# Kernel tuning notes

Measured on AMD Instinct MI355X. Metric: run time of the kernel, lower is better.

Reference implementation:

```python
import jax, jax.numpy as jnp
import numpy as np

EPS = 1e-8


def _cdist(a, b):
    # a: [B,N,3], b: [B,M,3] -> euclidean distances [B,N,M]
    a2 = jnp.sum(a * a, axis=-1)[:, :, None]          # [B,N,1]
    b2 = jnp.sum(b * b, axis=-1)[:, None, :]          # [B,1,M]
    ab = jnp.einsum('bnd,bmd->bnm', a, b)             # [B,N,M]
    d2 = jnp.maximum(a2 + b2 - 2.0 * ab, 0.0)
    return jnp.sqrt(d2)


def setup_inputs() -> dict:
    key = jax.random.key(0)
    ks = jax.random.split(key, 8)
    B, N, M, C1, C2 = 16, 4096, 1024, 128, 256
    Cin = C1 + C2  # 384
    H1, H2 = 256, 128
    return {
        'xyz1': jax.random.normal(ks[0], (B, N, 3), dtype=jnp.float32),
        'xyz2': jax.random.normal(ks[1], (B, M, 3), dtype=jnp.float32),
        'points1': jax.random.normal(ks[2], (B, C1, N), dtype=jnp.float32),
        'points2': jax.random.normal(ks[3], (B, C2, M), dtype=jnp.float32),
        'W1': jax.random.normal(ks[4], (H1, Cin), dtype=jnp.float32) * (1.0 / np.sqrt(Cin)),
        'b1': jnp.zeros((H1,), dtype=jnp.float32),
        'W2': jax.random.normal(ks[5], (H2, H1), dtype=jnp.float32) * (1.0 / np.sqrt(H1)),
        'b2': jnp.zeros((H2,), dtype=jnp.float32),
    }


def reference(xyz1, xyz2, points1, points2, W1, b1, W2, b2):
    # inverse-distance weighted interpolation over ALL M source points
    dist = _cdist(xyz1, xyz2) + EPS                   # [B,N,M]
    inv = 1.0 / dist
    weight = inv / jnp.sum(inv, axis=-1, keepdims=True)
    # interpolated features: [B,N,M] @ [B,M,C2] -> [B,C2,N]
    interpolated = jnp.einsum('bnm,bcm->bcn', weight, points2)
    new_points = jnp.concatenate([points1, interpolated], axis=1)  # [B,C1+C2,N]
    # 1x1 Conv1d MLP with ReLU
    h = jax.nn.relu(jnp.einsum('oc,bcn->bon', W1, new_points) + b1[None, :, None])
    out = jax.nn.relu(jnp.einsum('oc,bcn->bon', W2, h) + b2[None, :, None])
    return out
```

## Files before the change

### kernel.cpp

```cpp
#include <hip/hip_runtime.h>
#include <math.h>

#define BBATCH 16
#define NPTS   4096
#define MPTS   1024
#define C1c    128
#define C2c    256
#define CINc   384
#define H1c    256
#define H2c    128
#define TN     64

typedef _Float16 f16x8 __attribute__((ext_vector_type(8)));
typedef _Float16 f16x4 __attribute__((ext_vector_type(4)));
typedef float    f32x4 __attribute__((ext_vector_type(4)));

#define LDP2 40
#define LDXc 408
#define LDH  264

#define OFF_XYZ2 0
#define OFF_P2   12288
#define SMEM_BYTES 53248

#define WS_P2H  0
#define WS_W1H  (BBATCH * C2c * MPTS)
#define WS_W2H  (WS_W1H + H1c * CINc)
#define WS_F16_TOTAL (WS_W2H + H2c * H1c)

__global__ __launch_bounds__(256) void cvt_f16(
    const float* __restrict__ p2, const float* __restrict__ W1,
    const float* __restrict__ W2, _Float16* __restrict__ ws)
{
    const int NP2 = BBATCH * C2c * MPTS / 4;
    const int NW1 = H1c * CINc / 4;
    const int i = blockIdx.x * 256 + threadIdx.x;
    float4 v; _Float16* dst;
    if (i < NP2)            { v = ((const float4*)p2)[i];            dst = ws + WS_P2H + (size_t)i * 4; }
    else if (i < NP2 + NW1) { int j = i - NP2; v = ((const float4*)W1)[j]; dst = ws + WS_W1H + (size_t)j * 4; }
    else                    { int j = i - NP2 - NW1; v = ((const float4*)W2)[j]; dst = ws + WS_W2H + (size_t)j * 4; }
    f16x4 h;
    h[0] = (_Float16)v.x; h[1] = (_Float16)v.y; h[2] = (_Float16)v.z; h[3] = (_Float16)v.w;
    *(f16x4*)dst = h;
}

template <bool F16P>
__global__ __launch_bounds__(256, 3) void fp_mfma2(
    const float* __restrict__ xyz1, const float* __restrict__ xyz2,
    const float* __restrict__ p1,   const float* __restrict__ p2,
    const float* __restrict__ W1,   const float* __restrict__ b1v,
    const float* __restrict__ W2,   const float* __restrict__ b2v,
    const _Float16* __restrict__ p2h, const _Float16* __restrict__ W1h,
    const _Float16* __restrict__ W2h,
    float* __restrict__ out)
{
    __shared__ __align__(16) char smem[SMEM_BYTES];
    float*    s_xyz2 = (float*)(smem + OFF_XYZ2);
    _Float16* s_p2   = (_Float16*)(smem + OFF_P2);
    _Float16* s_X    = (_Float16*)smem;
    _Float16* s_H    = (_Float16*)smem;

    const int tid  = threadIdx.x;
    const int w    = tid >> 6;
    const int L    = tid & 63;
    const int quad = L >> 4;
    const int l16  = L & 15;

    const int id = blockIdx.x;
    const int b  = (id & 7) * 2 + ((id >> 3) & 1);
    const int n0 = (id >> 4) * TN;

    const float*    __restrict__ p2b  = p2  + (size_t)b * C2c * MPTS;
    const _Float16* __restrict__ p2hb = F16P ? (p2h + (size_t)b * C2c * MPTS) : (const _Float16*)nullptr;
    const float*    __restrict__ z2b  = xyz2 + (size_t)b * MPTS * 3;

    for (int i = tid; i < MPTS * 3; i += 256) s_xyz2[i] = z2b[i];

    {
    }
    const float x1x = xyz1[((size_t)b * NPTS + n0 + w * 16 + l16) * 3 + 0];
    const float x1y = xyz1[((size_t)b * NPTS + n0 + w * 16 + l16) * 3 + 1];
    const float x1z = xyz1[((size_t)b * NPTS + n0 + w * 16 + l16) * 3 + 2];

    f32x4 acc[16];
    #pragma unroll
    for (int ct = 0; ct < 16; ++ct) acc[ct] = (f32x4){0.f, 0.f, 0.f, 0.f};
    f32x4 accS = (f32x4){0.f, 0.f, 0.f, 0.f};

    f16x8 onesv;
    #pragma unroll
    for (int i = 0; i < 8; ++i) onesv[i] = (_Float16)1.0f;

    f16x8  stg16[4];
    float4 stg32[8];

    if (F16P) {
        #pragma unroll
        for (int r = 0; r < 4; ++r)
            stg16[r] = *(const f16x8*)(p2hb + (size_t)(r * 64 + (tid >> 2)) * MPTS + (tid & 3) * 8);
    } else {
        #pragma unroll
        for (int r = 0; r < 8; ++r)
            stg32[r] = *(const float4*)(p2b + (size_t)(r * 32 + (tid >> 3)) * MPTS + (tid & 7) * 4);
    }

    __syncthreads();

    #pragma unroll 2
    for (int s = 0; s < 32; ++s) {
        _Float16* buf = s_p2 + (s & 1) * (C2c * LDP2);
        if (F16P) {
            #pragma unroll
            for (int r = 0; r < 4; ++r)
                *(f16x8*)(buf + (r * 64 + (tid >> 2)) * LDP2 + (tid & 3) * 8) = stg16[r];
        } else {
            #pragma unroll
            for (int r = 0; r < 8; ++r) {
                const float4 v = stg32[r];
                f16x4 h;
                h[0] = (_Float16)v.x; h[1] = (_Float16)v.y; h[2] = (_Float16)v.z; h[3] = (_Float16)v.w;
                *(f16x4*)(buf + (r * 32 + (tid >> 3)) * LDP2 + (tid & 7) * 4) = h;
            }
        }
        __syncthreads();

        if (s + 1 < 32) {
            const int m1 = (s + 1) * 32;
            if (F16P) {
                #pragma unroll
                for (int r = 0; r < 4; ++r)
                    stg16[r] = *(const f16x8*)(p2hb + (size_t)(r * 64 + (tid >> 2)) * MPTS + m1 + (tid & 3) * 8);
            } else {
                #pragma unroll
                for (int r = 0; r < 8; ++r)
                    stg32[r] = *(const float4*)(p2b + (size_t)(r * 32 + (tid >> 3)) * MPTS + m1 + (tid & 7) * 4);
            }
        }

        f32x4 zr[6];
        {
            const float* zp = s_xyz2 + (s * 32 + quad * 8) * 3;
            #pragma unroll
            for (int j = 0; j < 6; ++j) zr[j] = *(const f32x4*)(zp + j * 4);
        }
        const float* zv = (const float*)zr;
        f16x8 af;
        #pragma unroll
        for (int i = 0; i < 8; ++i) {
            const float dx = x1x - zv[3 * i + 0];
            const float dy = x1y - zv[3 * i + 1];
            const float dz = x1z - zv[3 * i + 2];
            const float d2 = fmaf(dx, dx, fmaf(dy, dy, fmaf(dz, dz, 1e-12f)));
            af[i] = (_Float16)__builtin_amdgcn_rsqf(d2);
        }

        accS = __builtin_amdgcn_mfma_f32_16x16x32_f16(af, onesv, accS, 0, 0, 0);
        const _Float16* bbase = buf + l16 * LDP2 + quad * 8;
        #pragma unroll
        for (int ct = 0; ct < 16; ++ct) {
            const f16x8 bf = *(const f16x8*)(bbase + ct * (16 * LDP2));
            acc[ct] = __builtin_amdgcn_mfma_f32_16x16x32_f16(af, bf, acc[ct], 0, 0, 0);
        }
    }

    __syncthreads();

    float rn[4];
    #pragma unroll
    for (int r = 0; r < 4; ++r) rn[r] = 1.0f / accS[r];

    #pragma unroll
    for (int ct = 0; ct < 16; ++ct)
        #pragma unroll
        for (int r = 0; r < 4; ++r)
            s_X[(w * 16 + quad * 4 + r) * LDXc + 128 + ct * 16 + l16] =
                (_Float16)(acc[ct][r] * rn[r]);

    {
        const float* p1b = p1 + (size_t)b * C1c * NPTS + n0;
        #pragma unroll
        for (int cc = 0; cc < 8; ++cc) {
            const int c = w * 32 + cc * 4;
            f16x4 v;
            v[0] = (_Float16)p1b[(size_t)(c + 0) * NPTS + L];
            v[1] = (_Float16)p1b[(size_t)(c + 1) * NPTS + L];
            v[2] = (_Float16)p1b[(size_t)(c + 2) * NPTS + L];
            v[3] = (_Float16)p1b[(size_t)(c + 3) * NPTS + L];
            *(f16x4*)(&s_X[L * LDXc + c]) = v;
        }
    }
    __syncthreads();

    f32x4 hacc[4][4];
    #pragma unroll
    for (int ct = 0; ct < 4; ++ct)
        #pragma unroll
        for (int nt = 0; nt < 4; ++nt)
            hacc[ct][nt] = (f32x4){0.f, 0.f, 0.f, 0.f};

    #pragma unroll 2
    for (int kc = 0; kc < 12; ++kc) {
        f16x8 af[4];
        if (F16P) {
            const _Float16* wp = W1h + (size_t)(w * 64 + l16) * CINc + kc * 32 + quad * 8;
            #pragma unroll
            for (int ct = 0; ct < 4; ++ct) af[ct] = *(const f16x8*)(wp + ct * (16 * CINc));
        } else {
            const float* wp = W1 + (size_t)(w * 64 + l16) * CINc + kc * 32 + quad * 8;
            #pragma unroll
            for (int ct = 0; ct < 4; ++ct) {
                const float4 a0 = *(const float4*)(wp + ct * (16 * CINc));
                const float4 a1 = *(const float4*)(wp + ct * (16 * CINc) + 4);
                f16x8 h;
                h[0] = (_Float16)a0.x; h[1] = (_Float16)a0.y; h[2] = (_Float16)a0.z; h[3] = (_Float16)a0.w;
                h[4] = (_Float16)a1.x; h[5] = (_Float16)a1.y; h[6] = (_Float16)a1.z; h[7] = (_Float16)a1.w;
                af[ct] = h;
            }
        }
        #pragma unroll
        for (int nt = 0; nt < 4; ++nt) {
            const f16x8 bf = *(const f16x8*)(&s_X[(nt * 16 + l16) * LDXc + kc * 32 + quad * 8]);
            #pragma unroll
            for (int ct = 0; ct < 4; ++ct)
                hacc[ct][nt] = __builtin_amdgcn_mfma_f32_16x16x32_f16(af[ct], bf, hacc[ct][nt], 0, 0, 0);
        }
    }

    __syncthreads();

    {
        f32x4 bb[4];
        #pragma unroll
        for (int ct = 0; ct < 4; ++ct)
            bb[ct] = *(const f32x4*)(b1v + w * 64 + ct * 16 + quad * 4);
        #pragma unroll
        for (int ct = 0; ct < 4; ++ct)
            #pragma unroll
            for (int nt = 0; nt < 4; ++nt) {
                const f32x4 v = hacc[ct][nt];
                f16x4 hv;
                hv[0] = (_Float16)fmaxf(v[0] + bb[ct][0], 0.f);
                hv[1] = (_Float16)fmaxf(v[1] + bb[ct][1], 0.f);
                hv[2] = (_Float16)fmaxf(v[2] + bb[ct][2], 0.f);
                hv[3] = (_Float16)fmaxf(v[3] + bb[ct][3], 0.f);
                *(f16x4*)(&s_H[(nt * 16 + l16) * LDH + w * 64 + ct * 16 + quad * 4]) = hv;
            }
    }
    __syncthreads();

    f32x4 oacc[2][4];
    #pragma unroll
    for (int ct = 0; ct < 2; ++ct)
        #pragma unroll
        for (int nt = 0; nt < 4; ++nt)
            oacc[ct][nt] = (f32x4){0.f, 0.f, 0.f, 0.f};

    #pragma unroll 2
    for (int oc = 0; oc < 8; ++oc) {
        f16x8 af2[2];
        if (F16P) {
            const _Float16* wp = W2h + (size_t)(w * 32 + l16) * H1c + oc * 32 + quad * 8;
            #pragma unroll
            for (int ct = 0; ct < 2; ++ct) af2[ct] = *(const f16x8*)(wp + ct * (16 * H1c));
        } else {
            const float* wp = W2 + (size_t)(w * 32 + l16) * H1c + oc * 32 + quad * 8;
            #pragma unroll
            for (int ct = 0; ct < 2; ++ct) {
                const float4 a0 = *(const float4*)(wp + ct * (16 * H1c));
                const float4 a1 = *(const float4*)(wp + ct * (16 * H1c) + 4);
                f16x8 h;
                h[0] = (_Float16)a0.x; h[1] = (_Float16)a0.y; h[2] = (_Float16)a0.z; h[3] = (_Float16)a0.w;
                h[4] = (_Float16)a1.x; h[5] = (_Float16)a1.y; h[6] = (_Float16)a1.z; h[7] = (_Float16)a1.w;
                af2[ct] = h;
            }
        }
        #pragma unroll
        for (int nt = 0; nt < 4; ++nt) {
            const f16x8 bf = *(const f16x8*)(&s_H[(nt * 16 + l16) * LDH + oc * 32 + quad * 8]);
            #pragma unroll
            for (int ct = 0; ct < 2; ++ct)
                oacc[ct][nt] = __builtin_amdgcn_mfma_f32_16x16x32_f16(af2[ct], bf, oacc[ct][nt], 0, 0, 0);
        }
    }

    {
        f32x4 bb2[2];
        #pragma unroll
        for (int ct = 0; ct < 2; ++ct)
            bb2[ct] = *(const f32x4*)(b2v + w * 32 + ct * 16 + quad * 4);
        #pragma unroll
        for (int ct = 0; ct < 2; ++ct)
            #pragma unroll
            for (int nt = 0; nt < 4; ++nt) {
                float* op = out + ((size_t)b * H2c + w * 32 + ct * 16 + quad * 4) * NPTS
                                + n0 + nt * 16 + l16;
                #pragma unroll
                for (int j = 0; j < 4; ++j)
                    op[(size_t)j * NPTS] = fmaxf(oacc[ct][nt][j] + bb2[ct][j], 0.f);
            }
    }
}

extern "C" void kernel_launch(void* const* d_in, const int* in_sizes, int n_in,
                              void* d_out, int out_size, void* d_ws, size_t ws_size,
                              hipStream_t stream) {
    (void)in_sizes; (void)n_in; (void)out_size;
    const float* xyz1 = (const float*)d_in[0];
    const float* xyz2 = (const float*)d_in[1];
    const float* p1   = (const float*)d_in[2];
    const float* p2   = (const float*)d_in[3];
    const float* W1   = (const float*)d_in[4];
    const float* b1   = (const float*)d_in[5];
    const float* W2   = (const float*)d_in[6];
    const float* b2   = (const float*)d_in[7];
    float* out = (float*)d_out;

    const bool useh = (ws_size >= (size_t)WS_F16_TOTAL * 2);
    dim3 grid(BBATCH * (NPTS / TN));
    dim3 block(256);
    if (useh) {
        _Float16* ws = (_Float16*)d_ws;
        const int ncvt = (BBATCH * C2c * MPTS + H1c * CINc + H2c * H1c) / 4;
        cvt_f16<<<dim3(ncvt / 256), dim3(256), 0, stream>>>(p2, W1, W2, ws);
        fp_mfma2<true><<<grid, block, 0, stream>>>(xyz1, xyz2, p1, p2, W1, b1, W2, b2,
                                                   ws + WS_P2H, ws + WS_W1H, ws + WS_W2H, out);
    } else {
        fp_mfma2<false><<<grid, block, 0, stream>>>(xyz1, xyz2, p1, p2, W1, b1, W2, b2,
                                                    nullptr, nullptr, nullptr, out);
    }
}
```

Before: 198.0 us.

## Swap MFMA operand roles: stream points2 from global, stage inverse weights in LDS

The interpolation GEMM is reorganized so each wave owns 64 output channels and loads its points2 A-fragments straight from global memory into registers, double-buffered. Only the 64x32 inverse-distance tile goes through LDS, which replaces staging the 256x32 points2 tile there. The row sums move from an extra MFMA against a ones vector to scalar accumulation plus a small LDS reduction. LDS traffic per step drops, at the cost of more redundant global/L2 reads of points2 across waves and blocks and a less coalesced access pattern.

```diff
diff --git a/kernel.cpp b/kernel.cpp
--- a/kernel.cpp
+++ b/kernel.cpp
@@ -15,12 +15,14 @@
 typedef _Float16 f16x4 __attribute__((ext_vector_type(4)));
 typedef float    f32x4 __attribute__((ext_vector_type(4)));
 
-#define LDP2 40
+#define LDI  40
 #define LDXc 408
 #define LDH  264
 
-#define OFF_XYZ2 0
-#define OFF_P2   12288
+#define OFF_XYZ2  0
+#define OFF_INV   12288
+#define OFF_RED   22528
+#define OFF_RECIP 52224
 #define SMEM_BYTES 53248
 
 #define WS_P2H  0
@@ -45,7 +47,7 @@
 }
 
 template <bool F16P>
-__global__ __launch_bounds__(256, 3) void fp_mfma2(
+__global__ __launch_bounds__(256, 3) void fp_mfma3(
     const float* __restrict__ xyz1, const float* __restrict__ xyz2,
     const float* __restrict__ p1,   const float* __restrict__ p2,
     const float* __restrict__ W1,   const float* __restrict__ b1v,
@@ -55,10 +57,12 @@
     float* __restrict__ out)
 {
     __shared__ __align__(16) char smem[SMEM_BYTES];
-    float*    s_xyz2 = (float*)(smem + OFF_XYZ2);
-    _Float16* s_p2   = (_Float16*)(smem + OFF_P2);
-    _Float16* s_X    = (_Float16*)smem;
-    _Float16* s_H    = (_Float16*)smem;
+    float*    s_xyz2  = (float*)(smem + OFF_XYZ2);
+    _Float16* s_inv   = (_Float16*)(smem + OFF_INV);
+    float*    s_red   = (float*)(smem + OFF_RED);
+    float*    s_recip = (float*)(smem + OFF_RECIP);
+    _Float16* s_X     = (_Float16*)smem;
+    _Float16* s_H     = (_Float16*)smem;
 
     const int tid  = threadIdx.x;
     const int w    = tid >> 6;
@@ -74,108 +78,139 @@
     const _Float16* __restrict__ p2hb = F16P ? (p2h + (size_t)b * C2c * MPTS) : (const _Float16*)nullptr;
     const float*    __restrict__ z2b  = xyz2 + (size_t)b * MPTS * 3;
 
-    for (int i = tid; i < MPTS * 3; i += 256) s_xyz2[i] = z2b[i];
-
-    {
-    }
-    const float x1x = xyz1[((size_t)b * NPTS + n0 + w * 16 + l16) * 3 + 0];
-    const float x1y = xyz1[((size_t)b * NPTS + n0 + w * 16 + l16) * 3 + 1];
-    const float x1z = xyz1[((size_t)b * NPTS + n0 + w * 16 + l16) * 3 + 2];
-
-    f32x4 acc[16];
+    for (int i = tid; i < MPTS * 3 / 4; i += 256)
+        ((f32x4*)s_xyz2)[i] = ((const f32x4*)z2b)[i];
+
+    const float x1x = xyz1[((size_t)b * NPTS + n0 + L) * 3 + 0];
+    const float x1y = xyz1[((size_t)b * NPTS + n0 + L) * 3 + 1];
+    const float x1z = xyz1[((size_t)b * NPTS + n0 + L) * 3 + 2];
+
+    f32x4 acc[4][4];
     #pragma unroll
-    for (int ct = 0; ct < 16; ++ct) acc[ct] = (f32x4){0.f, 0.f, 0.f, 0.f};
-    f32x4 accS = (f32x4){0.f, 0.f, 0.f, 0.f};
-
-    f16x8 onesv;
-    #pragma unroll
-    for (int i = 0; i < 8; ++i) onesv[i] = (_Float16)1.0f;
-
-    f16x8  stg16[4];
-    float4 stg32[8];
+    for (int ct = 0; ct < 4; ++ct)
+        #pragma unroll
+        for (int nt = 0; nt < 4; ++nt)
+            acc[ct][nt] = (f32x4){0.f, 0.f, 0.f, 0.f};
+
+    float ssum = 0.f;
+
+    const _Float16* aphb = F16P ? (p2hb + (size_t)(w * 64 + l16) * MPTS + quad * 8) : (const _Float16*)nullptr;
+    const float*    apfb = p2b + (size_t)(w * 64 + l16) * MPTS + quad * 8;
+
+    f16x8 Aa[2][4];
+
+    __syncthreads();
 
     if (F16P) {
         #pragma unroll
-        for (int r = 0; r < 4; ++r)
-            stg16[r] = *(const f16x8*)(p2hb + (size_t)(r * 64 + (tid >> 2)) * MPTS + (tid & 3) * 8);
+        for (int ct = 0; ct < 4; ++ct) Aa[0][ct] = *(const f16x8*)(aphb + ct * (16 * MPTS));
     } else {
         #pragma unroll
-        for (int r = 0; r < 8; ++r)
-            stg32[r] = *(const float4*)(p2b + (size_t)(r * 32 + (tid >> 3)) * MPTS + (tid & 7) * 4);
-    }
-
-    __syncthreads();
-
-    #pragma unroll 2
-    for (int s = 0; s < 32; ++s) {
-        _Float16* buf = s_p2 + (s & 1) * (C2c * LDP2);
-        if (F16P) {
-            #pragma unroll
-            for (int r = 0; r < 4; ++r)
-                *(f16x8*)(buf + (r * 64 + (tid >> 2)) * LDP2 + (tid & 3) * 8) = stg16[r];
-        } else {
-            #pragma unroll
-            for (int r = 0; r < 8; ++r) {
-                const float4 v = stg32[r];
-                f16x4 h;
-                h[0] = (_Float16)v.x; h[1] = (_Float16)v.y; h[2] = (_Float16)v.z; h[3] = (_Float16)v.w;
-                *(f16x4*)(buf + (r * 32 + (tid >> 3)) * LDP2 + (tid & 7) * 4) = h;
-            }
-        }
-        __syncthreads();
-
-        if (s + 1 < 32) {
-            const int m1 = (s + 1) * 32;
-            if (F16P) {
-                #pragma unroll
-                for (int r = 0; r < 4; ++r)
-                    stg16[r] = *(const f16x8*)(p2hb + (size_t)(r * 64 + (tid >> 2)) * MPTS + m1 + (tid & 3) * 8);
-            } else {
-                #pragma unroll
-                for (int r = 0; r < 8; ++r)
-                    stg32[r] = *(const float4*)(p2b + (size_t)(r * 32 + (tid >> 3)) * MPTS + m1 + (tid & 7) * 4);
-            }
-        }
-
+        for (int ct = 0; ct < 4; ++ct) {
+            const float4 a0 = *(const float4*)(apfb + ct * (16 * MPTS));
+            const float4 a1 = *(const float4*)(apfb + ct * (16 * MPTS) + 4);
+            f16x8 h;
+            h[0] = (_Float16)a0.x; h[1] = (_Float16)a0.y; h[2] = (_Float16)a0.z; h[3] = (_Float16)a0.w;
+            h[4] = (_Float16)a1.x; h[5] = (_Float16)a1.y; h[6] = (_Float16)a1.z; h[7] = (_Float16)a1.w;
+            Aa[0][ct] = h;
+        }
+    }
+    {
+        const float* zp = s_xyz2 + (w * 8) * 3;
         f32x4 zr[6];
-        {
-            const float* zp = s_xyz2 + (s * 32 + quad * 8) * 3;
-            #pragma unroll
-            for (int j = 0; j < 6; ++j) zr[j] = *(const f32x4*)(zp + j * 4);
-        }
+        #pragma unroll
+        for (int j = 0; j < 6; ++j) zr[j] = ((const f32x4*)zp)[j];
         const float* zv = (const float*)zr;
-        f16x8 af;
+        f16x8 iv;
         #pragma unroll
         for (int i = 0; i < 8; ++i) {
             const float dx = x1x - zv[3 * i + 0];
             const float dy = x1y - zv[3 * i + 1];
             const float dz = x1z - zv[3 * i + 2];
             const float d2 = fmaf(dx, dx, fmaf(dy, dy, fmaf(dz, dz, 1e-12f)));
-            af[i] = (_Float16)__builtin_amdgcn_rsqf(d2);
-        }
-
-        accS = __builtin_amdgcn_mfma_f32_16x16x32_f16(af, onesv, accS, 0, 0, 0);
-        const _Float16* bbase = buf + l16 * LDP2 + quad * 8;
-        #pragma unroll
-        for (int ct = 0; ct < 16; ++ct) {
-            const f16x8 bf = *(const f16x8*)(bbase + ct * (16 * LDP2));
-            acc[ct] = __builtin_amdgcn_mfma_f32_16x16x32_f16(af, bf, acc[ct], 0, 0, 0);
-        }
-    }
-
-    __syncthreads();
-
-    float rn[4];
-    #pragma unroll
-    for (int r = 0; r < 4; ++r) rn[r] = 1.0f / accS[r];
-
-    #pragma unroll
-    for (int ct = 0; ct < 16; ++ct)
-        #pragma unroll
-        for (int r = 0; r < 4; ++r)
-            s_X[(w * 16 + quad * 4 + r) * LDXc + 128 + ct * 16 + l16] =
-                (_Float16)(acc[ct][r] * rn[r]);
-
+            const float inv = __builtin_amdgcn_rsqf(d2);
+            ssum += inv;
+            iv[i] = (_Float16)inv;
+        }
+        *(f16x8*)(s_inv + L * LDI + w * 8) = iv;
+    }
+    __syncthreads();
+
+    #pragma unroll 2
+    for (int s = 0; s < 32; ++s) {
+        const int cur = s & 1;
+        if (s + 1 < 32) {
+            if (F16P) {
+                const _Float16* ap = aphb + (s + 1) * 32;
+                #pragma unroll
+                for (int ct = 0; ct < 4; ++ct) Aa[cur ^ 1][ct] = *(const f16x8*)(ap + ct * (16 * MPTS));
+            } else {
+                const float* ap = apfb + (s + 1) * 32;
+                #pragma unroll
+                for (int ct = 0; ct < 4; ++ct) {
+                    const float4 a0 = *(const float4*)(ap + ct * (16 * MPTS));
+                    const float4 a1 = *(const float4*)(ap + ct * (16 * MPTS) + 4);
+                    f16x8 h;
+                    h[0] = (_Float16)a0.x; h[1] = (_Float16)a0.y; h[2] = (_Float16)a0.z; h[3] = (_Float16)a0.w;
+                    h[4] = (_Float16)a1.x; h[5] = (_Float16)a1.y; h[6] = (_Float16)a1.z; h[7] = (_Float16)a1.w;
+                    Aa[cur ^ 1][ct] = h;
+                }
+            }
+        }
+        if (s + 1 < 32) {
+            const float* zp = s_xyz2 + ((s + 1) * 32 + w * 8) * 3;
+            f32x4 zr[6];
+            #pragma unroll
+            for (int j = 0; j < 6; ++j) zr[j] = ((const f32x4*)zp)[j];
+            const float* zv = (const float*)zr;
+            f16x8 iv;
+            #pragma unroll
+            for (int i = 0; i < 8; ++i) {
+                const float dx = x1x - zv[3 * i + 0];
+                const float dy = x1y - zv[3 * i + 1];
+                const float dz = x1z - zv[3 * i + 2];
+                const float d2 = fmaf(dx, dx, fmaf(dy, dy, fmaf(dz, dz, 1e-12f)));
+                const float inv = __builtin_amdgcn_rsqf(d2);
+                ssum += inv;
+                iv[i] = (_Float16)inv;
+            }
+            *(f16x8*)(s_inv + (cur ^ 1) * (64 * LDI) + L * LDI + w * 8) = iv;
+        }
+        const _Float16* bb = s_inv + cur * (64 * LDI) + l16 * LDI + quad * 8;
+        #pragma unroll
+        for (int nt = 0; nt < 4; ++nt) {
+            const f16x8 bf = *(const f16x8*)(bb + nt * (16 * LDI));
+            #pragma unroll
+            for (int ct = 0; ct < 4; ++ct)
+                acc[ct][nt] = __builtin_amdgcn_mfma_f32_16x16x32_f16(Aa[cur][ct], bf, acc[ct][nt], 0, 0, 0);
+        }
+        __syncthreads();
+    }
+
+    s_red[tid] = ssum;
+    __syncthreads();
+    if (tid < 64)
+        s_recip[tid] = 1.0f / (s_red[tid] + s_red[tid + 64] + s_red[tid + 128] + s_red[tid + 192]);
+    __syncthreads();
+
+    {
+        float rn4[4];
+        #pragma unroll
+        for (int nt = 0; nt < 4; ++nt) rn4[nt] = s_recip[nt * 16 + l16];
+        #pragma unroll
+        for (int ct = 0; ct < 4; ++ct)
+            #pragma unroll
+            for (int nt = 0; nt < 4; ++nt) {
+                const f32x4 v = acc[ct][nt];
+                const float r = rn4[nt];
+                f16x4 hv;
+                hv[0] = (_Float16)(v[0] * r);
+                hv[1] = (_Float16)(v[1] * r);
+                hv[2] = (_Float16)(v[2] * r);
+                hv[3] = (_Float16)(v[3] * r);
+                *(f16x4*)(&s_X[(nt * 16 + l16) * LDXc + 128 + w * 64 + ct * 16 + quad * 4]) = hv;
+            }
+    }
     {
         const float* p1b = p1 + (size_t)b * C1c * NPTS + n0;
         #pragma unroll
@@ -322,10 +357,10 @@
         _Float16* ws = (_Float16*)d_ws;
         const int ncvt = (BBATCH * C2c * MPTS + H1c * CINc + H2c * H1c) / 4;
         cvt_f16<<<dim3(ncvt / 256), dim3(256), 0, stream>>>(p2, W1, W2, ws);
-        fp_mfma2<true><<<grid, block, 0, stream>>>(xyz1, xyz2, p1, p2, W1, b1, W2, b2,
+        fp_mfma3<true><<<grid, block, 0, stream>>>(xyz1, xyz2, p1, p2, W1, b1, W2, b2,
                                                    ws + WS_P2H, ws + WS_W1H, ws + WS_W2H, out);
     } else {
-        fp_mfma2<false><<<grid, block, 0, stream>>>(xyz1, xyz2, p1, p2, W1, b1, W2, b2,
+        fp_mfma3<false><<<grid, block, 0, stream>>>(xyz1, xyz2, p1, p2, W1, b1, W2, b2,
                                                     nullptr, nullptr, nullptr, out);
     }
 }
```

New measurement: 216.2 us. 1.09x slower.

## Load points2 fragments directly from global and split waves over channels and points

Applied to the files above, without the earlier changes.

Removes the LDS double-buffered staging of points2 and its per-step barrier. Each wave now reads its MFMA A-operand fragments for points2 straight from global memory. The four waves are regrouped as 2 channel halves by 2 point halves, so each wave computes two 16-point weight tiles against 8 channel tiles, and the operand roles are transposed (features become A, weights become B). This cuts LDS traffic and synchronisation at the cost of more global or L2 reads per block and duplicated weight computation across channel-half waves. The interpolated output is written to shared memory in a transposed layout using f16x4 stores.

```diff
diff --git a/kernel.cpp b/kernel.cpp
--- a/kernel.cpp
+++ b/kernel.cpp
@@ -15,13 +15,9 @@
 typedef _Float16 f16x4 __attribute__((ext_vector_type(4)));
 typedef float    f32x4 __attribute__((ext_vector_type(4)));
 
-#define LDP2 40
 #define LDXc 408
 #define LDH  264
-
-#define OFF_XYZ2 0
-#define OFF_P2   12288
-#define SMEM_BYTES 53248
+#define SMEM_BYTES 52224
 
 #define WS_P2H  0
 #define WS_W1H  (BBATCH * C2c * MPTS)
@@ -45,7 +41,7 @@
 }
 
 template <bool F16P>
-__global__ __launch_bounds__(256, 3) void fp_mfma2(
+__global__ __launch_bounds__(256, 3) void fp_mfma5(
     const float* __restrict__ xyz1, const float* __restrict__ xyz2,
     const float* __restrict__ p1,   const float* __restrict__ p2,
     const float* __restrict__ W1,   const float* __restrict__ b1v,
@@ -55,8 +51,7 @@
     float* __restrict__ out)
 {
     __shared__ __align__(16) char smem[SMEM_BYTES];
-    float*    s_xyz2 = (float*)(smem + OFF_XYZ2);
-    _Float16* s_p2   = (_Float16*)(smem + OFF_P2);
+    float*    s_xyz2 = (float*)smem;
     _Float16* s_X    = (_Float16*)smem;
     _Float16* s_H    = (_Float16*)smem;
 
@@ -65,6 +60,8 @@
     const int L    = tid & 63;
     const int quad = L >> 4;
     const int l16  = L & 15;
+    const int wc   = w & 1;
+    const int wn   = w >> 1;
 
     const int id = blockIdx.x;
     const int b  = (id & 7) * 2 + ((id >> 3) & 1);
@@ -74,108 +71,110 @@
     const _Float16* __restrict__ p2hb = F16P ? (p2h + (size_t)b * C2c * MPTS) : (const _Float16*)nullptr;
     const float*    __restrict__ z2b  = xyz2 + (size_t)b * MPTS * 3;
 
-    for (int i = tid; i < MPTS * 3; i += 256) s_xyz2[i] = z2b[i];
-
-    {
-    }
-    const float x1x = xyz1[((size_t)b * NPTS + n0 + w * 16 + l16) * 3 + 0];
-    const float x1y = xyz1[((size_t)b * NPTS + n0 + w * 16 + l16) * 3 + 1];
-    const float x1z = xyz1[((size_t)b * NPTS + n0 + w * 16 + l16) * 3 + 2];
-
-    f32x4 acc[16];
-    #pragma unroll
-    for (int ct = 0; ct < 16; ++ct) acc[ct] = (f32x4){0.f, 0.f, 0.f, 0.f};
-    f32x4 accS = (f32x4){0.f, 0.f, 0.f, 0.f};
+    for (int i = tid; i < MPTS * 3 / 4; i += 256)
+        ((f32x4*)s_xyz2)[i] = ((const f32x4*)z2b)[i];
+
+    float qx[2], qy[2], qz[2];
+    #pragma unroll
+    for (int nt = 0; nt < 2; ++nt) {
+        const float* q = xyz1 + ((size_t)b * NPTS + n0 + wn * 32 + nt * 16 + l16) * 3;
+        qx[nt] = q[0]; qy[nt] = q[1]; qz[nt] = q[2];
+    }
+
+    f32x4 acc[8][2];
+    #pragma unroll
+    for (int ct = 0; ct < 8; ++ct)
+        #pragma unroll
+        for (int nt = 0; nt < 2; ++nt)
+            acc[ct][nt] = (f32x4){0.f, 0.f, 0.f, 0.f};
+    f32x4 accS[2];
+    accS[0] = (f32x4){0.f, 0.f, 0.f, 0.f};
+    accS[1] = (f32x4){0.f, 0.f, 0.f, 0.f};
 
     f16x8 onesv;
     #pragma unroll
     for (int i = 0; i < 8; ++i) onesv[i] = (_Float16)1.0f;
 
-    f16x8  stg16[4];
-    float4 stg32[8];
-
-    if (F16P) {
-        #pragma unroll
-        for (int r = 0; r < 4; ++r)
-            stg16[r] = *(const f16x8*)(p2hb + (size_t)(r * 64 + (tid >> 2)) * MPTS + (tid & 3) * 8);
-    } else {
-        #pragma unroll
-        for (int r = 0; r < 8; ++r)
-            stg32[r] = *(const float4*)(p2b + (size_t)(r * 32 + (tid >> 3)) * MPTS + (tid & 7) * 4);
-    }
+    const _Float16* aph = F16P ? (p2hb + (size_t)(wc * 128 + l16) * MPTS + quad * 8) : (const _Float16*)nullptr;
+    const float*    apf = p2b + (size_t)(wc * 128 + l16) * MPTS + quad * 8;
 
     __syncthreads();
 
     #pragma unroll 2
     for (int s = 0; s < 32; ++s) {
-        _Float16* buf = s_p2 + (s & 1) * (C2c * LDP2);
-        if (F16P) {
-            #pragma unroll
-            for (int r = 0; r < 4; ++r)
-                *(f16x8*)(buf + (r * 64 + (tid >> 2)) * LDP2 + (tid & 3) * 8) = stg16[r];
-        } else {
-            #pragma unroll
-            for (int r = 0; r < 8; ++r) {
-                const float4 v = stg32[r];
-                f16x4 h;
-                h[0] = (_Float16)v.x; h[1] = (_Float16)v.y; h[2] = (_Float16)v.z; h[3] = (_Float16)v.w;
-                *(f16x4*)(buf + (r * 32 + (tid >> 3)) * LDP2 + (tid & 7) * 4) = h;
-            }
-        }
-        __syncthreads();
-
-        if (s + 1 < 32) {
-            const int m1 = (s + 1) * 32;
-            if (F16P) {
-                #pragma unroll
-                for (int r = 0; r < 4; ++r)
-                    stg16[r] = *(const f16x8*)(p2hb + (size_t)(r * 64 + (tid >> 2)) * MPTS + m1 + (tid & 3) * 8);
-            } else {
-                #pragma unroll
-                for (int r = 0; r < 8; ++r)
-                    stg32[r] = *(const float4*)(p2b + (size_t)(r * 32 + (tid >> 3)) * MPTS + m1 + (tid & 7) * 4);
-            }
-        }
-
         f32x4 zr[6];
         {
             const float* zp = s_xyz2 + (s * 32 + quad * 8) * 3;
             #pragma unroll
-            for (int j = 0; j < 6; ++j) zr[j] = *(const f32x4*)(zp + j * 4);
+            for (int j = 0; j < 6; ++j) zr[j] = ((const f32x4*)zp)[j];
         }
         const float* zv = (const float*)zr;
-        f16x8 af;
+        f16x8 bf[2];
         #pragma unroll
         for (int i = 0; i < 8; ++i) {
-            const float dx = x1x - zv[3 * i + 0];
-            const float dy = x1y - zv[3 * i + 1];
-            const float dz = x1z - zv[3 * i + 2];
-            const float d2 = fmaf(dx, dx, fmaf(dy, dy, fmaf(dz, dz, 1e-12f)));
-            af[i] = (_Float16)__builtin_amdgcn_rsqf(d2);
-        }
-
-        accS = __builtin_amdgcn_mfma_f32_16x16x32_f16(af, onesv, accS, 0, 0, 0);
-        const _Float16* bbase = buf + l16 * LDP2 + quad * 8;
-        #pragma unroll
-        for (int ct = 0; ct < 16; ++ct) {
-            const f16x8 bf = *(const f16x8*)(bbase + ct * (16 * LDP2));
-            acc[ct] = __builtin_amdgcn_mfma_f32_16x16x32_f16(af, bf, acc[ct], 0, 0, 0);
-        }
-    }
-
-    __syncthreads();
-
-    float rn[4];
-    #pragma unroll
-    for (int r = 0; r < 4; ++r) rn[r] = 1.0f / accS[r];
-
-    #pragma unroll
-    for (int ct = 0; ct < 16; ++ct)
-        #pragma unroll
-        for (int r = 0; r < 4; ++r)
-            s_X[(w * 16 + quad * 4 + r) * LDXc + 128 + ct * 16 + l16] =
-                (_Float16)(acc[ct][r] * rn[r]);
-
+            const float mx = zv[3 * i + 0];
+            const float my = zv[3 * i + 1];
+            const float mz = zv[3 * i + 2];
+            #pragma unroll
+            for (int nt = 0; nt < 2; ++nt) {
+                const float dx = qx[nt] - mx;
+                const float dy = qy[nt] - my;
+                const float dz = qz[nt] - mz;
+                const float d2 = fmaf(dx, dx, fmaf(dy, dy, fmaf(dz, dz, 1e-12f)));
+                bf[nt][i] = (_Float16)__builtin_amdgcn_rsqf(d2);
+            }
+        }
+        #pragma unroll
+        for (int nt = 0; nt < 2; ++nt)
+            accS[nt] = __builtin_amdgcn_mfma_f32_16x16x32_f16(onesv, bf[nt], accS[nt], 0, 0, 0);
+
+        #pragma unroll
+        for (int g = 0; g < 2; ++g) {
+            f16x8 af[4];
+            if (F16P) {
+                const _Float16* ap = aph + s * 32;
+                #pragma unroll
+                for (int ct = 0; ct < 4; ++ct)
+                    af[ct] = *(const f16x8*)(ap + (size_t)(g * 4 + ct) * (16 * MPTS));
+            } else {
+                const float* ap = apf + s * 32;
+                #pragma unroll
+                for (int ct = 0; ct < 4; ++ct) {
+                    const float4 a0 = *(const float4*)(ap + (size_t)(g * 4 + ct) * (16 * MPTS));
+                    const float4 a1 = *(const float4*)(ap + (size_t)(g * 4 + ct) * (16 * MPTS) + 4);
+                    f16x8 h;
+                    h[0] = (_Float16)a0.x; h[1] = (_Float16)a0.y; h[2] = (_Float16)a0.z; h[3] = (_Float16)a0.w;
+                    h[4] = (_Float16)a1.x; h[5] = (_Float16)a1.y; h[6] = (_Float16)a1.z; h[7] = (_Float16)a1.w;
+                    af[ct] = h;
+                }
+            }
+            #pragma unroll
+            for (int ct = 0; ct < 4; ++ct)
+                #pragma unroll
+                for (int nt = 0; nt < 2; ++nt)
+                    acc[g * 4 + ct][nt] =
+                        __builtin_amdgcn_mfma_f32_16x16x32_f16(af[ct], bf[nt], acc[g * 4 + ct][nt], 0, 0, 0);
+        }
+    }
+
+    const float rn0 = 1.0f / accS[0][0];
+    const float rn1 = 1.0f / accS[1][0];
+
+    __syncthreads();
+
+    #pragma unroll
+    for (int ct = 0; ct < 8; ++ct)
+        #pragma unroll
+        for (int nt = 0; nt < 2; ++nt) {
+            const f32x4 v = acc[ct][nt];
+            const float r = nt ? rn1 : rn0;
+            f16x4 hv;
+            hv[0] = (_Float16)(v[0] * r);
+            hv[1] = (_Float16)(v[1] * r);
+            hv[2] = (_Float16)(v[2] * r);
+            hv[3] = (_Float16)(v[3] * r);
+            *(f16x4*)(&s_X[(wn * 32 + nt * 16 + l16) * LDXc + 128 + wc * 128 + ct * 16 + quad * 4]) = hv;
+        }
     {
         const float* p1b = p1 + (size_t)b * C1c * NPTS + n0;
         #pragma unroll
@@ -322,10 +321,10 @@
         _Float16* ws = (_Float16*)d_ws;
         const int ncvt = (BBATCH * C2c * MPTS + H1c * CINc + H2c * H1c) / 4;
         cvt_f16<<<dim3(ncvt / 256), dim3(256), 0, stream>>>(p2, W1, W2, ws);
-        fp_mfma2<true><<<grid, block, 0, stream>>>(xyz1, xyz2, p1, p2, W1, b1, W2, b2,
+        fp_mfma5<true><<<grid, block, 0, stream>>>(xyz1, xyz2, p1, p2, W1, b1, W2, b2,
                                                    ws + WS_P2H, ws + WS_W1H, ws + WS_W2H, out);
     } else {
-        fp_mfma2<false><<<grid, block, 0, stream>>>(xyz1, xyz2, p1, p2, W1, b1, W2, b2,
+        fp_mfma5<false><<<grid, block, 0, stream>>>(xyz1, xyz2, p1, p2, W1, b1, W2, b2,
                                                     nullptr, nullptr, nullptr, out);
     }
 }
```

New measurement: 283.3 us. 43.1% more time.
